# Optimization experiments

Measured on AMD Instinct MI355X. Metric: run time of the kernel, lower is better.

The kernel has to match this reference:

```python
import jax, jax.numpy as jnp
import numpy as np

# --- constants matching init_kwargs ---
D = 768        # d_model (hidden)
H = 12         # attn heads
DK = D // H    # 64
F = 3072       # KANsize1
G = 5          # grid_size
K = 3          # spline_order
C = G + K      # spline coefficients per (out,in)
EPS = 1e-5
# efficient-kan grid: arange(-K, G+K+1)*h + grid_range[0], grid_range=[-1,1], h=2/G
GRID = jnp.arange(-K, G + K + 1, dtype=jnp.float32) * (2.0 / G) - 1.0  # (G+2K+1,)


def b_splines(x, grid, k):
    """x: (..., in) -> B-spline bases (..., in, G+K) via Cox-de Boor."""
    xe = x[..., None]
    bases = ((xe >= grid[:-1]) & (xe < grid[1:])).astype(x.dtype)
    for j in range(1, k + 1):
        bases = ((xe - grid[:-(j + 1)]) / (grid[j:-1] - grid[:-(j + 1)]) * bases[..., :-1]
                 + (grid[j + 1:] - xe) / (grid[j + 1:] - grid[1:-j]) * bases[..., 1:])
    return bases


def kan_linear(x, base_w, spline_w, scaler):
    # efficient-kan KANLinear: silu-base GEMM + scaled spline GEMM
    base = jnp.einsum('bsi,oi->bso', jax.nn.silu(x), base_w)
    B = b_splines(x, GRID, K)                      # (b, s, in, C)
    sw = spline_w * scaler[..., None]              # (out, in, C)
    spline = jnp.einsum('bsic,oic->bso', B, sw)
    return base + spline


def layernorm(x, g, b):
    m = jnp.mean(x, -1, keepdims=True)
    v = jnp.var(x, -1, keepdims=True)
    return (x - m) * jax.lax.rsqrt(v + EPS) * g + b


def setup_inputs() -> dict:
    key = jax.random.key(0)
    ks = jax.random.split(key, 12)
    Bt, S = 2, 2048
    x = jax.random.normal(ks[0], (Bt, S, D), jnp.float32)
    mask = jnp.ones((Bt, 1, 1, S), bool)  # accepted but unused, as in source
    s = 0.02
    return {
        'x': x, 'mask': mask,
        'ln1_g': jnp.ones((D,), jnp.float32), 'ln1_b': jnp.zeros((D,), jnp.float32),
        'wq': jax.random.normal(ks[1], (D, D), jnp.float32) * s, 'bq': jnp.zeros((D,), jnp.float32),
        'wk': jax.random.normal(ks[2], (D, D), jnp.float32) * s, 'bk': jnp.zeros((D,), jnp.float32),
        'wv': jax.random.normal(ks[3], (D, D), jnp.float32) * s, 'bv': jnp.zeros((D,), jnp.float32),
        'ln2_g': jnp.ones((D,), jnp.float32), 'ln2_b': jnp.zeros((D,), jnp.float32),
        'base_w1': jax.random.normal(ks[4], (F, D), jnp.float32) * s,
        'spline_w1': jax.random.normal(ks[5], (F, D, C), jnp.float32) * 0.1,
        'scaler1': jnp.ones((F, D), jnp.float32),
        'base_w2': jax.random.normal(ks[6], (D, F), jnp.float32) * s,
        'spline_w2': jax.random.normal(ks[7], (D, F, C), jnp.float32) * 0.1,
        'scaler2': jnp.ones((D, F), jnp.float32),
    }


def reference(x, mask, ln1_g, ln1_b, wq, bq, wk, bk, wv, bv, ln2_g, ln2_b,
              base_w1, spline_w1, scaler1, base_w2, spline_w2, scaler2):
    Bt, S, _ = x.shape
    # MultiHeadedAttention (pre-norm inside; mask unused in source; dropout=eval identity)
    xn = layernorm(x, ln1_g, ln1_b)
    q = (xn @ wq.T + bq).reshape(Bt, S, H, DK).transpose(0, 2, 1, 3)
    k = (xn @ wk.T + bk).reshape(Bt, S, H, DK).transpose(0, 2, 1, 3)
    v = (xn @ wv.T + bv).reshape(Bt, S, H, DK).transpose(0, 2, 1, 3)
    scores = jnp.einsum('bhqd,bhkd->bhqk', q, k) / jnp.sqrt(jnp.float32(DK))
    p = jax.nn.softmax(scores, axis=-1)
    attn = jnp.einsum('bhqk,bhkd->bhqd', p, v).transpose(0, 2, 1, 3).reshape(Bt, S, D)
    x = x + attn
    # SublayerConnection: x + KAN-FFN(norm(x))
    h = layernorm(x, ln2_g, ln2_b)
    h = kan_linear(h, base_w1, spline_w1, scaler1)
    h = kan_linear(h, base_w2, spline_w2, scaler2)
    return x + h
```

## Files before the change

kernel.cpp:

```cpp
#include <hip/hip_runtime.h>
#include <hip/hip_fp16.h>
#include <math.h>

#define DEV static __device__ __forceinline__

namespace {
constexpr int S  = 2048;
constexpr int D  = 768;
constexpr int Hh = 12;
constexpr int DK = 64;
constexpr int F  = 3072;
constexpr int Nn = 4096;
constexpr int FEAT = 9;
constexpr int K1   = D * FEAT;
constexpr int LDAB = 6912;
}

typedef _Float16 half8 __attribute__((ext_vector_type(8)));
typedef float f32x4 __attribute__((ext_vector_type(4)));

DEV void gld16(const void* g, void* l) {
    __builtin_amdgcn_global_load_lds((__attribute__((address_space(1))) void*)g,
                                     (__attribute__((address_space(3))) void*)l,
                                     16, 0, 0);
}

DEV void features9(float xv, float* f) {
    f[0] = xv / (1.0f + __expf(-xv));
    float sp = (xv + 2.2f) * 2.5f;
    float fj = floorf(sp);
    int j = (int)fj;
    float u = sp - fj;
    float u2 = u * u, u3 = u2 * u;
    float omu = 1.0f - u;
    float b0 = (1.0f / 6.0f) * omu * omu * omu;
    float b1 = 0.5f * u3 - u2 + (2.0f / 3.0f);
    float b2 = -0.5f * u3 + 0.5f * u2 + 0.5f * u + (1.0f / 6.0f);
    float b3 = (1.0f / 6.0f) * u3;
#pragma unroll
    for (int m = 0; m < 8; ++m) {
        int d = j - m;
        f[1 + m] = (d == 3) ? b0 : (d == 2) ? b1 : (d == 1) ? b2 : (d == 0) ? b3 : 0.0f;
    }
}

__global__ __launch_bounds__(256) void ln16_kernel(const float* __restrict__ x,
                                                   const float* __restrict__ g,
                                                   const float* __restrict__ bta,
                                                   _Float16* __restrict__ y) {
    int row = blockIdx.x;
    const float* xr = x + (size_t)row * D;
    _Float16* yr = y + (size_t)row * D;
    int t = threadIdx.x;
    float v[3];
#pragma unroll
    for (int j = 0; j < 3; ++j) v[j] = xr[t + j * 256];
    float s = v[0] + v[1] + v[2];
#pragma unroll
    for (int o = 1; o < 64; o <<= 1) s += __shfl_xor(s, o, 64);
    __shared__ float red[4], red2[4];
    int wid = t >> 6;
    if ((t & 63) == 0) red[wid] = s;
    __syncthreads();
    float mean = (red[0] + red[1] + red[2] + red[3]) * (1.0f / 768.0f);
    float d0 = v[0] - mean, d1 = v[1] - mean, d2 = v[2] - mean;
    float sq = d0 * d0 + d1 * d1 + d2 * d2;
#pragma unroll
    for (int o = 1; o < 64; o <<= 1) sq += __shfl_xor(sq, o, 64);
    if ((t & 63) == 0) red2[wid] = sq;
    __syncthreads();
    float var = (red2[0] + red2[1] + red2[2] + red2[3]) * (1.0f / 768.0f);
    float rstd = rsqrtf(var + 1e-5f);
#pragma unroll
    for (int j = 0; j < 3; ++j) {
        int c = t + j * 256;
        yr[c] = (_Float16)((v[j] - mean) * rstd * g[c] + bta[c]);
    }
}

__global__ __launch_bounds__(256) void ln_feat(const float* __restrict__ xa,
                                               const float* __restrict__ xb,
                                               const float* __restrict__ g,
                                               const float* __restrict__ bta,
                                               _Float16* __restrict__ feat) {
    int row = blockIdx.x;
    const float* xar = xa + (size_t)row * D;
    const float* xbr = xb + (size_t)row * D;
    int t = threadIdx.x;
    float v[3];
#pragma unroll
    for (int j = 0; j < 3; ++j) v[j] = xar[t + j * 256] + xbr[t + j * 256];
    float s = v[0] + v[1] + v[2];
#pragma unroll
    for (int o = 1; o < 64; o <<= 1) s += __shfl_xor(s, o, 64);
    __shared__ float red[4], red2[4];
    __shared__ __align__(16) _Float16 fbuf[K1];
    int wid = t >> 6;
    if ((t & 63) == 0) red[wid] = s;
    __syncthreads();
    float mean = (red[0] + red[1] + red[2] + red[3]) * (1.0f / 768.0f);
    float d0 = v[0] - mean, d1 = v[1] - mean, d2 = v[2] - mean;
    float sq = d0 * d0 + d1 * d1 + d2 * d2;
#pragma unroll
    for (int o = 1; o < 64; o <<= 1) sq += __shfl_xor(sq, o, 64);
    if ((t & 63) == 0) red2[wid] = sq;
    __syncthreads();
    float var = (red2[0] + red2[1] + red2[2] + red2[3]) * (1.0f / 768.0f);
    float rstd = rsqrtf(var + 1e-5f);
#pragma unroll
    for (int j = 0; j < 3; ++j) {
        int c = t + j * 256;
        float y = (v[j] - mean) * rstd * g[c] + bta[c];
        float f[9];
        features9(y, f);
#pragma unroll
        for (int cc = 0; cc < 9; ++cc) fbuf[c * 9 + cc] = (_Float16)f[cc];
    }
    __syncthreads();
    _Float16* dst = feat + (size_t)row * K1;
    for (int i = t; i < K1 / 8; i += 256)
        *(half8*)(dst + i * 8) = *(const half8*)&fbuf[i * 8];
}

__global__ __launch_bounds__(256) void feat2_chunk(const _Float16* __restrict__ h1,
                                                   int c0,
                                                   _Float16* __restrict__ feat) {
    int row = blockIdx.x;
    int t = threadIdx.x;
    __shared__ __align__(16) _Float16 fbuf[K1];
    const _Float16* src = h1 + (size_t)row * F + c0;
#pragma unroll
    for (int j = 0; j < 3; ++j) {
        int ic = t + j * 256;
        float y = (float)src[ic];
        float f[9];
        features9(y, f);
#pragma unroll
        for (int cc = 0; cc < 9; ++cc) fbuf[ic * 9 + cc] = (_Float16)f[cc];
    }
    __syncthreads();
    _Float16* dst = feat + (size_t)row * K1;
    for (int i = t; i < K1 / 8; i += 256)
        *(half8*)(dst + i * 8) = *(const half8*)&fbuf[i * 8];
}

__global__ __launch_bounds__(256) void prep_w(const float* __restrict__ bw,
                                              const float* __restrict__ sw,
                                              const float* __restrict__ scal,
                                              _Float16* __restrict__ Wp,
                                              int INfull, int c0) {
    int o = blockIdx.y;
    int ic = blockIdx.x * 256 + threadIdx.x;
    size_t idx = (size_t)o * INfull + c0 + ic;
    float bwv = bw[idx];
    float sc  = scal[idx];
    float4 s0 = *(const float4*)(sw + idx * 8);
    float4 s1 = *(const float4*)(sw + idx * 8 + 4);
    _Float16* dst = Wp + ((size_t)o * 768 + ic) * 9;
    dst[0] = (_Float16)bwv;
    dst[1] = (_Float16)(s0.x * sc);
    dst[2] = (_Float16)(s0.y * sc);
    dst[3] = (_Float16)(s0.z * sc);
    dst[4] = (_Float16)(s0.w * sc);
    dst[5] = (_Float16)(s1.x * sc);
    dst[6] = (_Float16)(s1.y * sc);
    dst[7] = (_Float16)(s1.z * sc);
    dst[8] = (_Float16)(s1.w * sc);
}

__global__ __launch_bounds__(256) void prep_qkv(const float* __restrict__ wq,
                                                const float* __restrict__ wk,
                                                const float* __restrict__ wv,
                                                _Float16* __restrict__ Wh) {
    int idx = blockIdx.x * 256 + threadIdx.x;
    const int per = D * D;
    if (idx >= 3 * per) return;
    int z = idx / per, rem = idx - z * per;
    const float* w = (z == 0) ? wq : (z == 1) ? wk : wv;
    Wh[idx] = (_Float16)w[rem];
}

__global__ __launch_bounds__(256, 2) void qkv16(const _Float16* __restrict__ Xh,
                                                const _Float16* __restrict__ Wh,
                                                const float* __restrict__ bq,
                                                const float* __restrict__ bk,
                                                const float* __restrict__ bv,
                                                _Float16* __restrict__ q,
                                                _Float16* __restrict__ k,
                                                _Float16* __restrict__ v) {
    int z = blockIdx.z;
    const _Float16* W = Wh + (size_t)z * D * D;
    const float* bias = (z == 0) ? bq : (z == 1) ? bk : bv;
    _Float16* out     = (z == 0) ? q  : (z == 1) ? k  : v;

    __shared__ __align__(16) _Float16 As[128][72];
    int t = threadIdx.x;
    int l = t & 63, w = t >> 6;
    int m0 = blockIdx.y * 128, o0 = blockIdx.x * 128;
    int wr = (w >> 1) * 64, wc = (w & 1) * 64;
    int lm = l & 15, lk = (l >> 4) * 8;
    int srow = t >> 1, sh = t & 1;

    f32x4 acc[4][4];
#pragma unroll
    for (int a = 0; a < 4; ++a)
#pragma unroll
        for (int b = 0; b < 4; ++b)
#pragma unroll
            for (int c = 0; c < 4; ++c) acc[a][b][c] = 0.0f;

    const _Float16* bp0 = W + (size_t)(o0 + wc + lm) * D + lk;

    for (int kt = 0; kt < D / 64; ++kt) {
        half8 ar[4];
#pragma unroll
        for (int i = 0; i < 4; ++i)
            ar[i] = *(const half8*)(Xh + (size_t)(m0 + srow) * D + kt * 64 + sh * 32 + i * 8);
        __syncthreads();
#pragma unroll
        for (int i = 0; i < 4; ++i)
            *(half8*)&As[srow][sh * 32 + i * 8] = ar[i];
        __syncthreads();
        half8 bfr[2][4];
#pragma unroll
        for (int kc = 0; kc < 2; ++kc)
#pragma unroll
            for (int nf = 0; nf < 4; ++nf)
                bfr[kc][nf] = *(const half8*)(bp0 + (size_t)nf * 16 * D + kt * 64 + kc * 32);
#pragma unroll
        for (int kc = 0; kc < 2; ++kc) {
            half8 a_[4];
#pragma unroll
            for (int mf = 0; mf < 4; ++mf)
                a_[mf] = *(const half8*)&As[wr + mf * 16 + lm][kc * 32 + lk];
#pragma unroll
            for (int mf = 0; mf < 4; ++mf)
#pragma unroll
                for (int nf = 0; nf < 4; ++nf)
                    acc[mf][nf] = __builtin_amdgcn_mfma_f32_16x16x32_f16(a_[mf], bfr[kc][nf], acc[mf][nf], 0, 0, 0);
        }
    }
    int r0 = m0 + wr + (l >> 4) * 4;
    int c0 = o0 + wc + lm;
#pragma unroll
    for (int mf = 0; mf < 4; ++mf)
#pragma unroll
        for (int nf = 0; nf < 4; ++nf) {
            int col = c0 + nf * 16;
            int hh = col >> 6, dd = col & 63;
            float bv_ = bias[col];
#pragma unroll
            for (int r = 0; r < 4; ++r) {
                int n = r0 + mf * 16 + r;
                int b = n >> 11, ss = n & 2047;
                out[(((size_t)(b * Hh + hh) * S + ss) * DK + dd)] = (_Float16)(acc[mf][nf][r] + bv_);
            }
        }
}

__global__ __launch_bounds__(256) void attn16(const _Float16* __restrict__ q16,
                                              const _Float16* __restrict__ k16,
                                              const _Float16* __restrict__ v16,
                                              float* __restrict__ attno) {
    int bh = blockIdx.y;
    int q0 = blockIdx.x * 64;
    int t = threadIdx.x;
    int l = t & 63, w = t >> 6;
    int lm = l & 15, lk = (l >> 4) * 8;
    int wr = w * 16;

    __shared__ __align__(16) _Float16 Qs[64][72];
    __shared__ __align__(16) _Float16 Ks[64][72];
    __shared__ __align__(16) _Float16 Vt[64][72];
    __shared__ __align__(16) _Float16 Ps[64][72];

    const _Float16* qb = q16 + ((size_t)bh * S + q0) * DK;
    const _Float16* kb = k16 + (size_t)bh * S * DK;
    const _Float16* vb = v16 + (size_t)bh * S * DK;

    {
        int row = t & 63, dg = t >> 6;
        half8 h0 = *(const half8*)(qb + row * DK + dg * 16);
        half8 h1 = *(const half8*)(qb + row * DK + dg * 16 + 8);
#pragma unroll
        for (int j = 0; j < 8; ++j) { h0[j] = h0[j] * (_Float16)0.125f; h1[j] = h1[j] * (_Float16)0.125f; }
        *(half8*)&Qs[row][dg * 16] = h0;
        *(half8*)&Qs[row][dg * 16 + 8] = h1;
    }

    float m_[4], l_[4];
    f32x4 oacc[4];
#pragma unroll
    for (int r = 0; r < 4; ++r) { m_[r] = -INFINITY; l_[r] = 0.0f; }
#pragma unroll
    for (int nf = 0; nf < 4; ++nf)
#pragma unroll
        for (int r = 0; r < 4; ++r) oacc[nf][r] = 0.0f;

    for (int kt = 0; kt < S / 64; ++kt) {
        __syncthreads();
        {
            int key = t & 63, dg = t >> 6;
            const _Float16* kr = kb + ((size_t)kt * 64 + key) * DK + dg * 16;
            half8 k0 = *(const half8*)(kr);
            half8 k1 = *(const half8*)(kr + 8);
            *(half8*)&Ks[key][dg * 16] = k0;
            *(half8*)&Ks[key][dg * 16 + 8] = k1;
            const _Float16* vr = vb + ((size_t)kt * 64 + key) * DK + dg * 16;
            half8 v0 = *(const half8*)(vr);
            half8 v1 = *(const half8*)(vr + 8);
#pragma unroll
            for (int j = 0; j < 8; ++j) {
                Vt[dg * 16 + j][key] = v0[j];
                Vt[dg * 16 + 8 + j][key] = v1[j];
            }
        }
        __syncthreads();

        f32x4 sc[4];
#pragma unroll
        for (int nf = 0; nf < 4; ++nf)
#pragma unroll
            for (int r = 0; r < 4; ++r) sc[nf][r] = 0.0f;
#pragma unroll
        for (int kc = 0; kc < 2; ++kc) {
            half8 aq = *(const half8*)&Qs[wr + lm][kc * 32 + lk];
#pragma unroll
            for (int nf = 0; nf < 4; ++nf) {
                half8 bk8 = *(const half8*)&Ks[nf * 16 + lm][kc * 32 + lk];
                sc[nf] = __builtin_amdgcn_mfma_f32_16x16x32_f16(aq, bk8, sc[nf], 0, 0, 0);
            }
        }
        float pmax[4];
#pragma unroll
        for (int r = 0; r < 4; ++r) {
            pmax[r] = fmaxf(fmaxf(sc[0][r], sc[1][r]), fmaxf(sc[2][r], sc[3][r]));
#pragma unroll
            for (int mk = 1; mk < 16; mk <<= 1)
                pmax[r] = fmaxf(pmax[r], __shfl_xor(pmax[r], mk, 64));
        }
        float corr[4], rs[4];
#pragma unroll
        for (int r = 0; r < 4; ++r) {
            float mnew = fmaxf(m_[r], pmax[r]);
            corr[r] = __expf(m_[r] - mnew);
            m_[r] = mnew;
            rs[r] = 0.0f;
        }
#pragma unroll
        for (int nf = 0; nf < 4; ++nf)
#pragma unroll
            for (int r = 0; r < 4; ++r) {
                float p = __expf(sc[nf][r] - m_[r]);
                sc[nf][r] = p;
                rs[r] += p;
            }
#pragma unroll
        for (int r = 0; r < 4; ++r) {
#pragma unroll
            for (int mk = 1; mk < 16; mk <<= 1)
                rs[r] += __shfl_xor(rs[r], mk, 64);
            l_[r] = l_[r] * corr[r] + rs[r];
        }
        int pr = wr + (l >> 4) * 4;
#pragma unroll
        for (int nf = 0; nf < 4; ++nf)
#pragma unroll
            for (int r = 0; r < 4; ++r)
                Ps[pr + r][nf * 16 + lm] = (_Float16)sc[nf][r];
#pragma unroll
        for (int nf = 0; nf < 4; ++nf)
#pragma unroll
            for (int r = 0; r < 4; ++r) oacc[nf][r] *= corr[r];
#pragma unroll
        for (int kc = 0; kc < 2; ++kc) {
            half8 ap = *(const half8*)&Ps[wr + lm][kc * 32 + lk];
#pragma unroll
            for (int nf = 0; nf < 4; ++nf) {
                half8 bv8 = *(const half8*)&Vt[nf * 16 + lm][kc * 32 + lk];
                oacc[nf] = __builtin_amdgcn_mfma_f32_16x16x32_f16(ap, bv8, oacc[nf], 0, 0, 0);
            }
        }
    }
    int b = bh / Hh, hh = bh % Hh;
    int pr = wr + (l >> 4) * 4;
#pragma unroll
    for (int r = 0; r < 4; ++r) {
        float inv = 1.0f / l_[r];
        float* orow = attno + ((size_t)b * S + q0 + pr + r) * D + hh * DK;
#pragma unroll
        for (int nf = 0; nf < 4; ++nf)
            orow[nf * 16 + lm] = oacc[nf][r] * inv;
    }
}

template <int KS, bool TOF16>
__global__ __launch_bounds__(256) void kan_gemm(const _Float16* __restrict__ A,
                                                const _Float16* __restrict__ B,
                                                _Float16* __restrict__ out16,
                                                float* __restrict__ out32,
                                                int O, int accum) {
    __shared__ __align__(16) _Float16 Al[128 * 64];
    __shared__ __align__(16) _Float16 Bl[128 * 64];
    int t = threadIdx.x;
    int l = t & 63, w = t >> 6;
    int m0 = blockIdx.y * 128, o0 = blockIdx.x * 128;
    int slot = blockIdx.z;
    int wr = (w >> 1) * 64, wc = (w & 1) * 64;
    int lm = l & 15, lk = (l >> 4) * 8;

    const _Float16* Ab = A + (size_t)slot * KS * 64;
    const _Float16* Bb = B + (size_t)slot * KS * 64;
    int srow = l >> 3, scol = (l & 7) * 8;

    f32x4 acc[4][4];
#pragma unroll
    for (int a = 0; a < 4; ++a)
#pragma unroll
        for (int b = 0; b < 4; ++b)
#pragma unroll
            for (int c = 0; c < 4; ++c) acc[a][b][c] = 0.0f;

    for (int kt = 0; kt < KS; ++kt) {
        if (kt) __syncthreads();
        size_t kofs = (size_t)kt * 64 + scol;
#pragma unroll
        for (int j = 0; j < 4; ++j) {
            int row = w * 32 + j * 8;
            gld16(Ab + (size_t)(m0 + row + srow) * LDAB + kofs, &Al[row * 64]);
            gld16(Bb + (size_t)(o0 + row + srow) * LDAB + kofs, &Bl[row * 64]);
        }
        __syncthreads();
#pragma unroll
        for (int kc = 0; kc < 2; ++kc) {
            half8 af[4], bf[4];
#pragma unroll
            for (int mf = 0; mf < 4; ++mf)
                af[mf] = *(const half8*)&Al[(wr + mf * 16 + lm) * 64 + kc * 32 + lk];
#pragma unroll
            for (int nf = 0; nf < 4; ++nf)
                bf[nf] = *(const half8*)&Bl[(wc + nf * 16 + lm) * 64 + kc * 32 + lk];
#pragma unroll
            for (int mf = 0; mf < 4; ++mf)
#pragma unroll
                for (int nf = 0; nf < 4; ++nf)
                    acc[mf][nf] = __builtin_amdgcn_mfma_f32_16x16x32_f16(af[mf], bf[nf], acc[mf][nf], 0, 0, 0);
        }
    }
    int r0 = m0 + wr + (l >> 4) * 4;
    int c0 = o0 + wc + lm;
#pragma unroll
    for (int mf = 0; mf < 4; ++mf)
#pragma unroll
        for (int nf = 0; nf < 4; ++nf)
#pragma unroll
            for (int r = 0; r < 4; ++r) {
                int row = r0 + mf * 16 + r;
                int col = c0 + nf * 16;
                if constexpr (TOF16) {
                    out16[(size_t)row * O + col] = (_Float16)acc[mf][nf][r];
                } else {
                    float* po = out32 + ((size_t)slot * Nn + row) * O + col;
                    float vv = acc[mf][nf][r];
                    if (accum) vv += *po;
                    *po = vv;
                }
            }
}

__global__ __launch_bounds__(256) void reduce4(const float* __restrict__ part,
                                               const float* __restrict__ x,
                                               const float* __restrict__ attno,
                                               float* __restrict__ out) {
    int i = blockIdx.x * 256 + threadIdx.x;
    const size_t ND4 = (size_t)Nn * D / 4;
    if (i >= (int)ND4) return;
    const float4* p0 = (const float4*)part;
    const float4* p1 = p0 + ND4;
    const float4* p2 = p1 + ND4;
    const float4* p3 = p2 + ND4;
    float4 a = p0[i], b = p1[i], c = p2[i], d = p3[i];
    float4 xe = ((const float4*)x)[i], at = ((const float4*)attno)[i];
    float4 o;
    o.x = a.x + b.x + c.x + d.x + xe.x + at.x;
    o.y = a.y + b.y + c.y + d.y + xe.y + at.y;
    o.z = a.z + b.z + c.z + d.z + xe.z + at.z;
    o.w = a.w + b.w + c.w + d.w + xe.w + at.w;
    ((float4*)out)[i] = o;
}

extern "C" void kernel_launch(void* const* d_in, const int* in_sizes, int n_in,
                              void* d_out, int out_size, void* d_ws, size_t ws_size,
                              hipStream_t stream) {
    const float* x    = (const float*)d_in[0];
    const float* ln1g = (const float*)d_in[2];
    const float* ln1b = (const float*)d_in[3];
    const float* wq   = (const float*)d_in[4];
    const float* bq   = (const float*)d_in[5];
    const float* wk   = (const float*)d_in[6];
    const float* bk   = (const float*)d_in[7];
    const float* wv   = (const float*)d_in[8];
    const float* bv   = (const float*)d_in[9];
    const float* ln2g = (const float*)d_in[10];
    const float* ln2b = (const float*)d_in[11];
    const float* bw1  = (const float*)d_in[12];
    const float* sw1  = (const float*)d_in[13];
    const float* sc1  = (const float*)d_in[14];
    const float* bw2  = (const float*)d_in[15];
    const float* sw2  = (const float*)d_in[16];
    const float* sc2  = (const float*)d_in[17];

    const size_t ND = (size_t)Nn * D;
    char* base = (char*)d_ws;
    _Float16* featbuf = (_Float16*)base;
    _Float16* q16 = featbuf;
    _Float16* k16 = featbuf + ND;
    _Float16* v16 = featbuf + 2 * ND;
    char* p = base + (size_t)Nn * K1 * 2;
    float* attno = (float*)p;            p += ND * 4;
    _Float16* h1h = (_Float16*)p;        p += (size_t)Nn * F * 2;
    char* R3 = p;
    _Float16* Wp1 = (_Float16*)R3;
    _Float16* xnh = (_Float16*)(R3 + 42467328);
    _Float16* Wh  = (_Float16*)(R3 + 48758784);
    float* part   = (float*)R3;
    char* R4 = R3 + 52297728;
    _Float16* Wp2c = (_Float16*)R4;

    ln16_kernel<<<Nn, 256, 0, stream>>>(x, ln1g, ln1b, xnh);
    prep_qkv<<<(3 * D * D + 255) / 256, 256, 0, stream>>>(wq, wk, wv, Wh);
    qkv16<<<dim3(D / 128, Nn / 128, 3), 256, 0, stream>>>(xnh, Wh, bq, bk, bv, q16, k16, v16);
    attn16<<<dim3(S / 64, 2 * Hh), 256, 0, stream>>>(q16, k16, v16, attno);
    prep_w<<<dim3(3, F), 256, 0, stream>>>(bw1, sw1, sc1, Wp1, D, 0);
    ln_feat<<<Nn, 256, 0, stream>>>(x, attno, ln2g, ln2b, featbuf);
    kan_gemm<108, true><<<dim3(F / 128, Nn / 128, 1), 256, 0, stream>>>(
        featbuf, Wp1, h1h, nullptr, F, 0);
    for (int c = 0; c < 4; ++c) {
        prep_w<<<dim3(3, D), 256, 0, stream>>>(bw2, sw2, sc2, Wp2c, F, c * 768);
        feat2_chunk<<<Nn, 256, 0, stream>>>(h1h, c * 768, featbuf);
        kan_gemm<27, false><<<dim3(D / 128, Nn / 128, 4), 256, 0, stream>>>(
            featbuf, Wp2c, nullptr, part, D, c > 0);
    }
    reduce4<<<(int)(ND / 4 / 256), 256, 0, stream>>>(part, x, attno, (float*)d_out);
}
```

Baseline: 1.133 ms.

## Swizzle workgroups across XCDs and enlarge attention tile to 128 queries

Adds an XCD-aware block-id remapping to the QKV, attention and KAN GEMM kernels so that workgroups sharing operands land on the same XCD and reuse its L2. The attention kernel moves to 512 threads and 128 query rows per block, which halves how often K/V tiles are reloaded, and splits K and V loading between the two halves of the block. It also raises wave priority around the MFMA sections. The cost is higher LDS and register pressure per attention block and fewer blocks in the attention grid.

```diff
diff --git a/kernel.cpp b/kernel.cpp
--- a/kernel.cpp
+++ b/kernel.cpp
@@ -23,6 +23,12 @@
     __builtin_amdgcn_global_load_lds((__attribute__((address_space(1))) void*)g,
                                      (__attribute__((address_space(3))) void*)l,
                                      16, 0, 0);
+}
+
+DEV int xcd_swz(int id, int nwg) {
+    int q = nwg >> 3, r = nwg & 7;
+    int xcd = id & 7, pos = id >> 3;
+    return (xcd < r ? xcd * (q + 1) : r * (q + 1) + (xcd - r) * q) + pos;
 }
 
 DEV void features9(float xv, float* f) {
@@ -188,7 +194,14 @@
                                                 _Float16* __restrict__ q,
                                                 _Float16* __restrict__ k,
                                                 _Float16* __restrict__ v) {
-    int z = blockIdx.z;
+    int nb = gridDim.x, mb = gridDim.y;
+    int nwg = nb * mb * gridDim.z;
+    int id = blockIdx.x + nb * (blockIdx.y + mb * blockIdx.z);
+    int id2 = xcd_swz(id, nwg);
+    int z = id2 / (nb * mb);
+    int rem = id2 % (nb * mb);
+    int m0 = (rem % mb) * 128, o0 = (rem / mb) * 128;
+
     const _Float16* W = Wh + (size_t)z * D * D;
     const float* bias = (z == 0) ? bq : (z == 1) ? bk : bv;
     _Float16* out     = (z == 0) ? q  : (z == 1) ? k  : v;
@@ -196,7 +209,6 @@
     __shared__ __align__(16) _Float16 As[128][72];
     int t = threadIdx.x;
     int l = t & 63, w = t >> 6;
-    int m0 = blockIdx.y * 128, o0 = blockIdx.x * 128;
     int wr = (w >> 1) * 64, wc = (w & 1) * 64;
     int lm = l & 15, lk = (l >> 4) * 8;
     int srow = t >> 1, sh = t & 1;
@@ -258,28 +270,32 @@
         }
 }
 
-__global__ __launch_bounds__(256) void attn16(const _Float16* __restrict__ q16,
+__global__ __launch_bounds__(512) void attn16(const _Float16* __restrict__ q16,
                                               const _Float16* __restrict__ k16,
                                               const _Float16* __restrict__ v16,
                                               float* __restrict__ attno) {
-    int bh = blockIdx.y;
-    int q0 = blockIdx.x * 64;
+    int nwg = gridDim.x * gridDim.y;
+    int id = blockIdx.x + gridDim.x * blockIdx.y;
+    int id2 = xcd_swz(id, nwg);
+    int bh = id2 / gridDim.x;
+    int q0 = (id2 % gridDim.x) * 128;
+
     int t = threadIdx.x;
     int l = t & 63, w = t >> 6;
     int lm = l & 15, lk = (l >> 4) * 8;
     int wr = w * 16;
 
-    __shared__ __align__(16) _Float16 Qs[64][72];
+    __shared__ __align__(16) _Float16 Qs[128][72];
+    __shared__ __align__(16) _Float16 Ps[128][72];
     __shared__ __align__(16) _Float16 Ks[64][72];
     __shared__ __align__(16) _Float16 Vt[64][72];
-    __shared__ __align__(16) _Float16 Ps[64][72];
 
     const _Float16* qb = q16 + ((size_t)bh * S + q0) * DK;
     const _Float16* kb = k16 + (size_t)bh * S * DK;
     const _Float16* vb = v16 + (size_t)bh * S * DK;
 
     {
-        int row = t & 63, dg = t >> 6;
+        int row = t >> 2, dg = t & 3;
         half8 h0 = *(const half8*)(qb + row * DK + dg * 16);
         half8 h1 = *(const half8*)(qb + row * DK + dg * 16 + 8);
 #pragma unroll
@@ -300,19 +316,23 @@
     for (int kt = 0; kt < S / 64; ++kt) {
         __syncthreads();
         {
-            int key = t & 63, dg = t >> 6;
-            const _Float16* kr = kb + ((size_t)kt * 64 + key) * DK + dg * 16;
-            half8 k0 = *(const half8*)(kr);
-            half8 k1 = *(const half8*)(kr + 8);
-            *(half8*)&Ks[key][dg * 16] = k0;
-            *(half8*)&Ks[key][dg * 16 + 8] = k1;
-            const _Float16* vr = vb + ((size_t)kt * 64 + key) * DK + dg * 16;
-            half8 v0 = *(const half8*)(vr);
-            half8 v1 = *(const half8*)(vr + 8);
-#pragma unroll
-            for (int j = 0; j < 8; ++j) {
-                Vt[dg * 16 + j][key] = v0[j];
-                Vt[dg * 16 + 8 + j][key] = v1[j];
+            int tt = t & 255;
+            int key = tt & 63, dg = tt >> 6;
+            if (t < 256) {
+                const _Float16* kr = kb + ((size_t)kt * 64 + key) * DK + dg * 16;
+                half8 k0 = *(const half8*)(kr);
+                half8 k1 = *(const half8*)(kr + 8);
+                *(half8*)&Ks[key][dg * 16] = k0;
+                *(half8*)&Ks[key][dg * 16 + 8] = k1;
+            } else {
+                const _Float16* vr = vb + ((size_t)kt * 64 + key) * DK + dg * 16;
+                half8 v0 = *(const half8*)(vr);
+                half8 v1 = *(const half8*)(vr + 8);
+#pragma unroll
+                for (int j = 0; j < 8; ++j) {
+                    Vt[dg * 16 + j][key] = v0[j];
+                    Vt[dg * 16 + 8 + j][key] = v1[j];
+                }
             }
         }
         __syncthreads();
@@ -322,6 +342,7 @@
         for (int nf = 0; nf < 4; ++nf)
 #pragma unroll
             for (int r = 0; r < 4; ++r) sc[nf][r] = 0.0f;
+        __builtin_amdgcn_s_setprio(1);
 #pragma unroll
         for (int kc = 0; kc < 2; ++kc) {
             half8 aq = *(const half8*)&Qs[wr + lm][kc * 32 + lk];
@@ -331,6 +352,7 @@
                 sc[nf] = __builtin_amdgcn_mfma_f32_16x16x32_f16(aq, bk8, sc[nf], 0, 0, 0);
             }
         }
+        __builtin_amdgcn_s_setprio(0);
         float pmax[4];
 #pragma unroll
         for (int r = 0; r < 4; ++r) {
@@ -372,6 +394,7 @@
         for (int nf = 0; nf < 4; ++nf)
 #pragma unroll
             for (int r = 0; r < 4; ++r) oacc[nf][r] *= corr[r];
+        __builtin_amdgcn_s_setprio(1);
 #pragma unroll
         for (int kc = 0; kc < 2; ++kc) {
             half8 ap = *(const half8*)&Ps[wr + lm][kc * 32 + lk];
@@ -381,6 +404,7 @@
                 oacc[nf] = __builtin_amdgcn_mfma_f32_16x16x32_f16(ap, bv8, oacc[nf], 0, 0, 0);
             }
         }
+        __builtin_amdgcn_s_setprio(0);
     }
     int b = bh / Hh, hh = bh % Hh;
     int pr = wr + (l >> 4) * 4;
@@ -402,10 +426,16 @@
                                                 int O, int accum) {
     __shared__ __align__(16) _Float16 Al[128 * 64];
     __shared__ __align__(16) _Float16 Bl[128 * 64];
+    int nb = gridDim.x, mb = gridDim.y;
+    int nwg = nb * mb * gridDim.z;
+    int id = blockIdx.x + nb * (blockIdx.y + mb * blockIdx.z);
+    int id2 = xcd_swz(id, nwg);
+    int slot = id2 / (nb * mb);
+    int rem = id2 % (nb * mb);
+    int m0 = (rem % mb) * 128, o0 = (rem / mb) * 128;
+
     int t = threadIdx.x;
     int l = t & 63, w = t >> 6;
-    int m0 = blockIdx.y * 128, o0 = blockIdx.x * 128;
-    int slot = blockIdx.z;
     int wr = (w >> 1) * 64, wc = (w & 1) * 64;
     int lm = l & 15, lk = (l >> 4) * 8;
 
@@ -530,7 +560,7 @@
     ln16_kernel<<<Nn, 256, 0, stream>>>(x, ln1g, ln1b, xnh);
     prep_qkv<<<(3 * D * D + 255) / 256, 256, 0, stream>>>(wq, wk, wv, Wh);
     qkv16<<<dim3(D / 128, Nn / 128, 3), 256, 0, stream>>>(xnh, Wh, bq, bk, bv, q16, k16, v16);
-    attn16<<<dim3(S / 64, 2 * Hh), 256, 0, stream>>>(q16, k16, v16, attno);
+    attn16<<<dim3(S / 128, 2 * Hh), 512, 0, stream>>>(q16, k16, v16, attno);
     prep_w<<<dim3(3, F), 256, 0, stream>>>(bw1, sw1, sc1, Wp1, D, 0);
     ln_feat<<<Nn, 256, 0, stream>>>(x, attno, ln2g, ln2b, featbuf);
     kan_gemm<108, true><<<dim3(F / 128, Nn / 128, 1), 256, 0, stream>>>(
```

After: 1.164 ms. 2.7% more time.
